# Performance work log

Measured on AMD Instinct MI355X. Metric: run time of the kernel, lower is better.

Reference implementation:

```python
import jax, jax.numpy as jnp
import numpy as np

N, LQ, C, M, L, P = 8, 2048, 256, 8, 4, 4
DH = C // M  # 32
LENS = (2048, 1024, 512, 256)


def setup_inputs() -> dict:
    key = jax.random.key(0)
    ks = jax.random.split(key, 8)
    s = 1.0 / np.sqrt(C)
    return {
        "query": jax.random.normal(ks[0], (N, LQ, C), jnp.float32),
        "reference_points": jax.random.uniform(ks[1], (N, LQ, L, 1), jnp.float32),
        "input_flatten": jax.random.normal(ks[2], (N, sum(LENS), C), jnp.float32),
        "temporal_lens": np.array(LENS, np.int64),
        "level_start_index": np.array([0, 2048, 3072, 3584], np.int64),
        "W_off": jax.random.normal(ks[3], (C, M * L * P), jnp.float32) * 0.01,
        "b_off": jax.random.normal(ks[4], (M * L * P,), jnp.float32),
        "W_attn": jax.random.normal(ks[5], (C, M * L * P), jnp.float32) * 0.01,
        "b_attn": jnp.zeros((M * L * P,), jnp.float32),
        "W_val": jax.random.normal(ks[6], (C, C), jnp.float32) * s,
        "b_val": jnp.zeros((C,), jnp.float32),
        "W_out": jax.random.normal(ks[7], (C, C), jnp.float32) * s,
        "b_out": jnp.zeros((C,), jnp.float32),
    }


def _deform_core(value, lens, loc, attn):
    # value: (N, S, M, DH); loc, attn: (N, LQ, M, L, P); loc in normalized [0,1] coords.
    # Equivalent to per-level F.grid_sample (bilinear, zeros padding, align_corners=False)
    # on a 1xT image: pixel position = loc*T - 0.5; the y-coord 0.5 lands exactly on row 0.
    outs = []
    start = 0
    for l, T in enumerate(lens):
        v = value[:, start:start + T].transpose(0, 2, 1, 3)  # (N, M, T, DH)
        start += T
        pos = loc[..., l, :] * T - 0.5                       # (N, LQ, M, P)
        x0f = jnp.floor(pos)
        frac = pos - x0f
        x0 = x0f.astype(jnp.int32)

        def gather(idx):
            i = jnp.clip(idx, 0, T - 1).transpose(0, 2, 1, 3).reshape(N, M, LQ * P, 1)
            return jnp.take_along_axis(v, i, axis=2).reshape(N, M, LQ, P, DH)

        in0 = ((x0 >= 0) & (x0 < T)).astype(value.dtype)
        in1 = ((x0 + 1 >= 0) & (x0 + 1 < T)).astype(value.dtype)
        w0 = ((1.0 - frac) * in0).transpose(0, 2, 1, 3)[..., None]  # (N, M, LQ, P, 1)
        w1 = (frac * in1).transpose(0, 2, 1, 3)[..., None]
        outs.append(gather(x0) * w0 + gather(x0 + 1) * w1)          # (N, M, LQ, P, DH)
    sampled = jnp.stack(outs, axis=3)          # (N, M, LQ, L, P, DH)
    aw = attn.transpose(0, 2, 1, 3, 4)         # (N, M, LQ, L, P)
    return jnp.einsum('nmqlpd,nmqlp->nqmd', sampled, aw).reshape(N, LQ, C)


def reference(query, reference_points, input_flatten, temporal_lens, level_start_index,
              W_off, b_off, W_attn, b_attn, W_val, b_val, W_out, b_out):
    lens = [int(t) for t in np.asarray(temporal_lens)[:L]]  # static per-level lengths
    value = (input_flatten @ W_val + b_val).reshape(N, -1, M, DH)
    off = (query @ W_off + b_off).reshape(N, LQ, M, L, P)
    attn = jax.nn.softmax((query @ W_attn + b_attn).reshape(N, LQ, M, L * P), axis=-1)
    attn = attn.reshape(N, LQ, M, L, P)
    norm = jnp.asarray(lens, query.dtype)                    # offset_normalizer (L,)
    loc = reference_points[:, :, None, :, None, 0] + off / norm[None, None, None, :, None]
    out = _deform_core(value, lens, loc, attn)
    out = out @ W_out + b_out
    return out, loc, attn
```

## Files before the change

kernel.cpp:

```cpp
#include <hip/hip_runtime.h>
#include <hip/hip_bf16.h>
#include <math.h>

#define NB 8
#define LQ 2048
#define CCH 256
#define SSUM 3840

typedef unsigned short ushort_t;
typedef unsigned int uint_t;
typedef __attribute__((ext_vector_type(8))) short bf16x8;
typedef __attribute__((ext_vector_type(4))) float f32x4;

__device__ inline ushort_t f2bf(float f) {
  __hip_bfloat16 h = __float2bfloat16(f);
  return *reinterpret_cast<ushort_t*>(&h);
}
__device__ inline uint_t pk2bf(float lo, float hi) {
  float2 t; t.x = lo; t.y = hi;
  __hip_bfloat162 h = __float22bfloat162_rn(t);
  return *reinterpret_cast<uint_t*>(&h);
}
__device__ inline float bf2f_lo(uint_t u) {
  union { uint_t u32; float f; } x;
  x.u32 = u << 16;
  return x.f;
}
__device__ inline float bf2f_hi(uint_t u) {
  union { uint_t u32; float f; } x;
  x.u32 = u & 0xffff0000u;
  return x.f;
}

__global__ __launch_bounds__(256) void gemm_multi(
    int job_base,
    const float* __restrict__ in_flat, const float* __restrict__ query,
    const ushort_t* __restrict__ core,
    const float* __restrict__ W_val, const float* __restrict__ W_off,
    const float* __restrict__ W_attn, const float* __restrict__ W_out,
    const float* __restrict__ b_val, const float* __restrict__ b_off,
    const float* __restrict__ b_attn, const float* __restrict__ b_out,
    ushort_t* __restrict__ value, float* __restrict__ loc,
    float* __restrict__ attn, float* __restrict__ out) {
  __shared__ ushort_t Abf[2][128][24];
  __shared__ ushort_t Bbf[2][128][24];

  const int job = job_base + blockIdx.x;

  const float* Af = nullptr;
  const ushort_t* Ab16 = nullptr;
  const float* W; const float* bias;
  int wstride, wcol, bm, cstride, colbase;
  float* Cf = nullptr; ushort_t* Cb = nullptr;

  if (job < 480) {
    int bn = (job & 1) * 128; bm = (job >> 1) * 128;
    Af = in_flat; W = W_val; wstride = 256; wcol = bn;
    bias = b_val + bn; Cb = value; cstride = 256; colbase = bn;
  } else if (job < 736) {
    int p = job - 480; bm = (p >> 1) * 128;
    Af = query;
    if (p & 1) { W = W_attn; bias = b_attn; Cf = attn; }
    else       { W = W_off;  bias = b_off;  Cf = loc;  }
    wstride = 128; wcol = 0; cstride = 128; colbase = 0;
  } else {
    int o = job - 736; int bn = (o & 1) * 128; bm = (o >> 1) * 128;
    Ab16 = core; W = W_out; wstride = 256; wcol = bn;
    bias = b_out + bn; Cf = out; cstride = 256; colbase = bn;
  }

  const int tid = threadIdx.x;
  const int lane = tid & 63;
  const int wv = tid >> 6;
  const int wm = (wv >> 1) * 64;
  const int wn = (wv & 1) * 64;
  const int quad = lane >> 4;
  const int l16 = lane & 15;
  const int sr = tid & 127;
  const int sh = tid >> 7;
  const int kq = tid >> 5;
  const int ln = tid & 31;

  f32x4 acc[4][4];
#pragma unroll
  for (int i = 0; i < 4; ++i)
#pragma unroll
    for (int j = 0; j < 4; ++j) acc[i][j] = (f32x4)(0.f);

  for (int k0 = 0; k0 < 256; k0 += 32) {
    uint4 aq0, aq1;
    if (Af) {
      const float* gp = Af + (size_t)(bm + sr) * 256 + k0 + sh * 16;
      float4 f0 = *(const float4*)(gp + 0);
      float4 f1 = *(const float4*)(gp + 4);
      float4 f2 = *(const float4*)(gp + 8);
      float4 f3 = *(const float4*)(gp + 12);
      aq0.x = pk2bf(f0.x, f0.y); aq0.y = pk2bf(f0.z, f0.w);
      aq0.z = pk2bf(f1.x, f1.y); aq0.w = pk2bf(f1.z, f1.w);
      aq1.x = pk2bf(f2.x, f2.y); aq1.y = pk2bf(f2.z, f2.w);
      aq1.z = pk2bf(f3.x, f3.y); aq1.w = pk2bf(f3.z, f3.w);
    } else {
      const ushort_t* gp = Ab16 + (size_t)(bm + sr) * 256 + k0 + sh * 16;
      aq0 = *(const uint4*)(gp + 0);
      aq1 = *(const uint4*)(gp + 8);
    }
    float wreg[16];
#pragma unroll
    for (int j = 0; j < 4; ++j) {
      const float* wp = W + (size_t)(k0 + kq + j * 8) * wstride + wcol + ln;
#pragma unroll
      for (int nb = 0; nb < 4; ++nb) wreg[j * 4 + nb] = wp[nb * 32];
    }

    __syncthreads();
    *(uint4*)&Abf[sh][sr][0] = aq0;
    *(uint4*)&Abf[sh][sr][8] = aq1;
#pragma unroll
    for (int j = 0; j < 4; ++j) {
      int k = kq + j * 8;
#pragma unroll
      for (int nb = 0; nb < 4; ++nb)
        Bbf[k >> 4][ln + nb * 32][k & 15] = f2bf(wreg[j * 4 + nb]);
    }
    __syncthreads();

    bf16x8 af[4], bfr[4];
#pragma unroll
    for (int mi = 0; mi < 4; ++mi)
      af[mi] = *(const bf16x8*)&Abf[quad >> 1][wm + mi * 16 + l16][(quad & 1) * 8];
#pragma unroll
    for (int ni = 0; ni < 4; ++ni)
      bfr[ni] = *(const bf16x8*)&Bbf[quad >> 1][wn + ni * 16 + l16][(quad & 1) * 8];
#pragma unroll
    for (int mi = 0; mi < 4; ++mi)
#pragma unroll
      for (int ni = 0; ni < 4; ++ni)
        acc[mi][ni] = __builtin_amdgcn_mfma_f32_16x16x32_bf16(af[mi], bfr[ni], acc[mi][ni], 0, 0, 0);
  }

#pragma unroll
  for (int ni = 0; ni < 4; ++ni) {
    int cc = wn + ni * 16 + l16;
    float bv = bias[cc];
#pragma unroll
    for (int mi = 0; mi < 4; ++mi) {
      f32x4 v = acc[mi][ni];
      int rbase = bm + wm + mi * 16 + quad * 4;
#pragma unroll
      for (int r = 0; r < 4; ++r) {
        float o = v[r] + bv;
        size_t idx = (size_t)(rbase + r) * cstride + colbase + cc;
        if (Cb) Cb[idx] = f2bf(o);
        else    Cf[idx] = o;
      }
    }
  }
}

__global__ __launch_bounds__(256) void deform_fused(
    const ushort_t* __restrict__ value,
    float* __restrict__ locbuf,
    float* __restrict__ attnbuf,
    const float* __restrict__ refp,
    ushort_t* __restrict__ core) {
  const int tid = threadIdx.x;
  const int nq0 = blockIdx.x * 4;
  const int n = nq0 >> 11;

  __shared__ float slv[512];
  __shared__ float slog[512];
  __shared__ float4 sp[512];

  const float rnorm[4] = {1.f / 2048.f, 1.f / 1024.f, 1.f / 512.f, 1.f / 256.f};
  const int lensA[4] = {2048, 1024, 512, 256};
  const int startsA[4] = {0, 2048, 3072, 3584};

#pragma unroll
  for (int j = 0; j < 2; ++j) {
    int s = tid + j * 256;
    int q = s >> 7;
    int r = s & 127;
    int l = (r >> 2) & 3;
    float lv = refp[(size_t)(nq0 + q) * 4 + l] +
               locbuf[(size_t)nq0 * 128 + s] * rnorm[l];
    locbuf[(size_t)nq0 * 128 + s] = lv;
    slv[s] = lv;
    slog[s] = attnbuf[(size_t)nq0 * 128 + s];
  }
  __syncthreads();

  if (tid < 32) {
    int base = tid * 16;
    float v[16];
#pragma unroll
    for (int i = 0; i < 16; ++i) v[i] = slog[base + i];
    float mx = v[0];
#pragma unroll
    for (int i = 1; i < 16; ++i) mx = fmaxf(mx, v[i]);
    float ssum = 0.f;
#pragma unroll
    for (int i = 0; i < 16; ++i) { v[i] = __expf(v[i] - mx); ssum += v[i]; }
    float rs = 1.f / ssum;
    float* gout = attnbuf + (size_t)nq0 * 128 + base;
#pragma unroll
    for (int i = 0; i < 16; ++i) {
      float pv = v[i] * rs;
      slog[base + i] = pv;
      gout[i] = pv;
    }
  }
  __syncthreads();

#pragma unroll
  for (int j = 0; j < 2; ++j) {
    int s = tid + j * 256;
    int q = s >> 7;
    int r = s & 127;
    int m = r >> 4;
    int lp = r & 15;
    int l = lp >> 2;
    int T = lensA[l];
    float lv = slv[s];
    float aw = slog[s];
    float pos = lv * (float)T - 0.5f;
    float x0f = floorf(pos);
    float fr = pos - x0f;
    int x0 = (int)x0f;
    float w0 = ((unsigned)x0 < (unsigned)T) ? (1.f - fr) * aw : 0.f;
    float w1 = ((unsigned)(x0 + 1) < (unsigned)T) ? fr * aw : 0.f;
    int i0 = min(max(x0, 0), T - 1);
    int i1 = min(max(x0 + 1, 0), T - 1);
    float4 pr;
    pr.x = w0;
    pr.y = w1;
    pr.z = __int_as_float((startsA[l] + i0) * 256);
    pr.w = __int_as_float((startsA[l] + i1) * 256);
    sp[q * 128 + lp * 8 + m] = pr;
  }
  __syncthreads();

  const int q = tid >> 6;
  const int t64 = tid & 63;
  const int m = t64 >> 3;
  const int g = t64 & 7;
  const ushort_t* vbase = value + (size_t)n * (SSUM * 256) + m * 32 + g * 4;

  float a0 = 0.f, a1 = 0.f, a2 = 0.f, a3 = 0.f;
#pragma unroll
  for (int lp = 0; lp < 16; ++lp) {
    float4 pr = sp[q * 128 + lp * 8 + m];
    int o0 = __float_as_int(pr.z);
    int o1 = __float_as_int(pr.w);
    uint2 u0 = *(const uint2*)(vbase + o0);
    uint2 u1 = *(const uint2*)(vbase + o1);
    a0 += pr.x * bf2f_lo(u0.x) + pr.y * bf2f_lo(u1.x);
    a1 += pr.x * bf2f_hi(u0.x) + pr.y * bf2f_hi(u1.x);
    a2 += pr.x * bf2f_lo(u0.y) + pr.y * bf2f_lo(u1.y);
    a3 += pr.x * bf2f_hi(u0.y) + pr.y * bf2f_hi(u1.y);
  }
  uint2 outp;
  outp.x = (uint_t)f2bf(a0) | ((uint_t)f2bf(a1) << 16);
  outp.y = (uint_t)f2bf(a2) | ((uint_t)f2bf(a3) << 16);
  *(uint2*)&core[(size_t)(nq0 + q) * 256 + m * 32 + g * 4] = outp;
}

extern "C" void kernel_launch(void* const* d_in, const int* in_sizes, int n_in,
                              void* d_out, int out_size, void* d_ws, size_t ws_size,
                              hipStream_t stream) {
  const float* query    = (const float*)d_in[0];
  const float* refpts   = (const float*)d_in[1];
  const float* in_flat  = (const float*)d_in[2];
  const float* W_off  = (const float*)d_in[5];
  const float* b_off  = (const float*)d_in[6];
  const float* W_attn = (const float*)d_in[7];
  const float* b_attn = (const float*)d_in[8];
  const float* W_val  = (const float*)d_in[9];
  const float* b_val  = (const float*)d_in[10];
  const float* W_out  = (const float*)d_in[11];
  const float* b_out  = (const float*)d_in[12];

  float* out  = (float*)d_out;
  float* loc  = out + (size_t)NB * LQ * CCH;
  float* attn = loc + (size_t)NB * LQ * 128;

  ushort_t* value = (ushort_t*)d_ws;
  ushort_t* core  = value + (size_t)NB * SSUM * CCH;

  const int Mq = NB * LQ;

  gemm_multi<<<736, 256, 0, stream>>>(
      0, in_flat, query, core, W_val, W_off, W_attn, W_out,
      b_val, b_off, b_attn, b_out, value, loc, attn, out);

  deform_fused<<<Mq / 4, 256, 0, stream>>>(value, loc, attn, refpts, core);

  gemm_multi<<<256, 256, 0, stream>>>(
      736, in_flat, query, core, W_val, W_off, W_attn, W_out,
      b_val, b_off, b_attn, b_out, value, loc, attn, out);
}
```

Before: 180.9 us.

## Pre-convert inputs and weights to bf16, use async global-to-LDS double-buffered GEMM

Adds a prologue kernel that converts in_flat and query to bf16 and writes transposed bf16 copies of all weight matrices. The GEMM kernel is replaced by one that streams bf16 tiles straight into LDS with global_load_lds, double-buffered, using a 64x128 tile in place of 128x128. The aim is to drop the in-loop fp32 loads, conversions and strided weight reads and to overlap loads with MFMA. The cost is an extra launch and an extra full read and write pass over the activations, and the core buffer now aliases the query_bf buffer.

```diff
diff --git a/kernel.cpp b/kernel.cpp
--- a/kernel.cpp
+++ b/kernel.cpp
@@ -4,7 +4,6 @@
 
 #define NB 8
 #define LQ 2048
-#define CCH 256
 #define SSUM 3840
 
 typedef unsigned short ushort_t;
@@ -12,127 +11,132 @@
 typedef __attribute__((ext_vector_type(8))) short bf16x8;
 typedef __attribute__((ext_vector_type(4))) float f32x4;
 
-__device__ inline ushort_t f2bf(float f) {
+__device__ __forceinline__ ushort_t f2bf(float f) {
   __hip_bfloat16 h = __float2bfloat16(f);
   return *reinterpret_cast<ushort_t*>(&h);
 }
-__device__ inline uint_t pk2bf(float lo, float hi) {
+__device__ __forceinline__ uint_t pk2bf(float lo, float hi) {
   float2 t; t.x = lo; t.y = hi;
   __hip_bfloat162 h = __float22bfloat162_rn(t);
   return *reinterpret_cast<uint_t*>(&h);
 }
-__device__ inline float bf2f_lo(uint_t u) {
+__device__ __forceinline__ float bf2f_lo(uint_t u) {
   union { uint_t u32; float f; } x;
   x.u32 = u << 16;
   return x.f;
 }
-__device__ inline float bf2f_hi(uint_t u) {
+__device__ __forceinline__ float bf2f_hi(uint_t u) {
   union { uint_t u32; float f; } x;
   x.u32 = u & 0xffff0000u;
   return x.f;
 }
-
-__global__ __launch_bounds__(256) void gemm_multi(
-    int job_base,
+__device__ __forceinline__ void ld_lds16(const void* g, void* l) {
+  __builtin_amdgcn_global_load_lds(
+      (const __attribute__((address_space(1))) void*)g,
+      (__attribute__((address_space(3))) void*)l, 16, 0, 0);
+}
+
+#define NF4A ((NB * SSUM * 256) / 4)
+#define NF4B ((NB * LQ * 256) / 4)
+
+__global__ __launch_bounds__(256) void prologue(
     const float* __restrict__ in_flat, const float* __restrict__ query,
-    const ushort_t* __restrict__ core,
     const float* __restrict__ W_val, const float* __restrict__ W_off,
     const float* __restrict__ W_attn, const float* __restrict__ W_out,
+    ushort_t* __restrict__ inflat_bf, ushort_t* __restrict__ query_bf,
+    ushort_t* __restrict__ BtVal, ushort_t* __restrict__ BtOA,
+    ushort_t* __restrict__ BtOut) {
+  const int b = blockIdx.x, t = threadIdx.x;
+  if (b < 256) { BtVal[b * 256 + t] = f2bf(W_val[(size_t)t * 256 + b]); return; }
+  if (b < 512) { int n = b - 256; BtOut[n * 256 + t] = f2bf(W_out[(size_t)t * 256 + n]); return; }
+  if (b < 640) { int n = b - 512; BtOA[n * 256 + t] = f2bf(W_off[(size_t)t * 128 + n]); return; }
+  if (b < 768) { int n = b - 640; BtOA[(128 + n) * 256 + t] = f2bf(W_attn[(size_t)t * 128 + n]); return; }
+  const int stride = (gridDim.x - 768) * 256;
+  for (int i = (b - 768) * 256 + t; i < NF4A + NF4B; i += stride) {
+    float4 v;
+    if (i < NF4A) v = ((const float4*)in_flat)[i];
+    else          v = ((const float4*)query)[i - NF4A];
+    uint2 o;
+    o.x = pk2bf(v.x, v.y);
+    o.y = pk2bf(v.z, v.w);
+    if (i < NF4A) *(uint2*)&inflat_bf[(size_t)i * 4] = o;
+    else          *(uint2*)&query_bf[(size_t)(i - NF4A) * 4] = o;
+  }
+}
+
+__global__ __launch_bounds__(256) void gemm_async(
+    int job_base,
+    const ushort_t* __restrict__ inflat_bf, const ushort_t* __restrict__ query_bf,
+    const ushort_t* __restrict__ core,
+    const ushort_t* __restrict__ BtVal, const ushort_t* __restrict__ BtOA,
+    const ushort_t* __restrict__ BtOut,
     const float* __restrict__ b_val, const float* __restrict__ b_off,
     const float* __restrict__ b_attn, const float* __restrict__ b_out,
     ushort_t* __restrict__ value, float* __restrict__ loc,
     float* __restrict__ attn, float* __restrict__ out) {
-  __shared__ ushort_t Abf[2][128][24];
-  __shared__ ushort_t Bbf[2][128][24];
+  __shared__ ushort_t Ab[2][64][32];
+  __shared__ ushort_t Bb[2][128][32];
 
   const int job = job_base + blockIdx.x;
 
-  const float* Af = nullptr;
-  const ushort_t* Ab16 = nullptr;
-  const float* W; const float* bias;
-  int wstride, wcol, bm, cstride, colbase;
-  float* Cf = nullptr; ushort_t* Cb = nullptr;
-
-  if (job < 480) {
-    int bn = (job & 1) * 128; bm = (job >> 1) * 128;
-    Af = in_flat; W = W_val; wstride = 256; wcol = bn;
-    bias = b_val + bn; Cb = value; cstride = 256; colbase = bn;
-  } else if (job < 736) {
-    int p = job - 480; bm = (p >> 1) * 128;
-    Af = query;
-    if (p & 1) { W = W_attn; bias = b_attn; Cf = attn; }
-    else       { W = W_off;  bias = b_off;  Cf = loc;  }
-    wstride = 128; wcol = 0; cstride = 128; colbase = 0;
+  const ushort_t* Asrc; const ushort_t* Bt; const float* bias;
+  int bm, colbase, cstride;
+  ushort_t* Cb = nullptr; float* Cf = nullptr;
+
+  if (job < 960) {
+    int cn = job & 1; bm = (job >> 1) * 64;
+    Asrc = inflat_bf; Bt = BtVal + cn * 128 * 256;
+    bias = b_val + cn * 128; Cb = value; cstride = 256; colbase = cn * 128;
+  } else if (job < 1472) {
+    int p = job - 960; int cn = p & 1; bm = (p >> 1) * 64;
+    Asrc = query_bf; Bt = BtOA + cn * 128 * 256;
+    bias = cn ? b_attn : b_off; Cf = cn ? attn : loc; cstride = 128; colbase = 0;
   } else {
-    int o = job - 736; int bn = (o & 1) * 128; bm = (o >> 1) * 128;
-    Ab16 = core; W = W_out; wstride = 256; wcol = bn;
-    bias = b_out + bn; Cf = out; cstride = 256; colbase = bn;
+    int o = job - 1472; int cn = o & 1; bm = (o >> 1) * 64;
+    Asrc = core; Bt = BtOut + cn * 128 * 256;
+    bias = b_out + cn * 128; Cf = out; cstride = 256; colbase = cn * 128;
   }
 
   const int tid = threadIdx.x;
   const int lane = tid & 63;
   const int wv = tid >> 6;
-  const int wm = (wv >> 1) * 64;
-  const int wn = (wv & 1) * 64;
   const int quad = lane >> 4;
   const int l16 = lane & 15;
-  const int sr = tid & 127;
-  const int sh = tid >> 7;
-  const int kq = tid >> 5;
-  const int ln = tid & 31;
-
-  f32x4 acc[4][4];
-#pragma unroll
-  for (int i = 0; i < 4; ++i)
+  const int wm = (wv >> 1) * 32;
+  const int wn = (wv & 1) * 64;
+  const int srow = lane >> 2;
+  const int skb = (lane & 3) * 8;
+
+  f32x4 acc[2][4];
+#pragma unroll
+  for (int i = 0; i < 2; ++i)
 #pragma unroll
     for (int j = 0; j < 4; ++j) acc[i][j] = (f32x4)(0.f);
 
-  for (int k0 = 0; k0 < 256; k0 += 32) {
-    uint4 aq0, aq1;
-    if (Af) {
-      const float* gp = Af + (size_t)(bm + sr) * 256 + k0 + sh * 16;
-      float4 f0 = *(const float4*)(gp + 0);
-      float4 f1 = *(const float4*)(gp + 4);
-      float4 f2 = *(const float4*)(gp + 8);
-      float4 f3 = *(const float4*)(gp + 12);
-      aq0.x = pk2bf(f0.x, f0.y); aq0.y = pk2bf(f0.z, f0.w);
-      aq0.z = pk2bf(f1.x, f1.y); aq0.w = pk2bf(f1.z, f1.w);
-      aq1.x = pk2bf(f2.x, f2.y); aq1.y = pk2bf(f2.z, f2.w);
-      aq1.z = pk2bf(f3.x, f3.y); aq1.w = pk2bf(f3.z, f3.w);
-    } else {
-      const ushort_t* gp = Ab16 + (size_t)(bm + sr) * 256 + k0 + sh * 16;
-      aq0 = *(const uint4*)(gp + 0);
-      aq1 = *(const uint4*)(gp + 8);
-    }
-    float wreg[16];
-#pragma unroll
-    for (int j = 0; j < 4; ++j) {
-      const float* wp = W + (size_t)(k0 + kq + j * 8) * wstride + wcol + ln;
-#pragma unroll
-      for (int nb = 0; nb < 4; ++nb) wreg[j * 4 + nb] = wp[nb * 32];
-    }
-
+  auto stage = [&](int db, int k0) {
+    ld_lds16(Asrc + (size_t)(bm + wv * 16 + srow) * 256 + k0 + skb,
+             &Ab[db][wv * 16 + srow][skb]);
+    ld_lds16(Bt + (size_t)(wv * 32 + srow) * 256 + k0 + skb,
+             &Bb[db][wv * 32 + srow][skb]);
+    ld_lds16(Bt + (size_t)(wv * 32 + 16 + srow) * 256 + k0 + skb,
+             &Bb[db][wv * 32 + 16 + srow][skb]);
+  };
+
+  stage(0, 0);
+#pragma unroll
+  for (int it = 0; it < 8; ++it) {
+    const int db = it & 1;
     __syncthreads();
-    *(uint4*)&Abf[sh][sr][0] = aq0;
-    *(uint4*)&Abf[sh][sr][8] = aq1;
-#pragma unroll
-    for (int j = 0; j < 4; ++j) {
-      int k = kq + j * 8;
-#pragma unroll
-      for (int nb = 0; nb < 4; ++nb)
-        Bbf[k >> 4][ln + nb * 32][k & 15] = f2bf(wreg[j * 4 + nb]);
-    }
-    __syncthreads();
-
-    bf16x8 af[4], bfr[4];
-#pragma unroll
-    for (int mi = 0; mi < 4; ++mi)
-      af[mi] = *(const bf16x8*)&Abf[quad >> 1][wm + mi * 16 + l16][(quad & 1) * 8];
+    if (it < 7) stage(db ^ 1, (it + 1) * 32);
+    bf16x8 af[2], bfr[4];
+#pragma unroll
+    for (int mi = 0; mi < 2; ++mi)
+      af[mi] = *(const bf16x8*)&Ab[db][wm + mi * 16 + l16][quad * 8];
 #pragma unroll
     for (int ni = 0; ni < 4; ++ni)
-      bfr[ni] = *(const bf16x8*)&Bbf[quad >> 1][wn + ni * 16 + l16][(quad & 1) * 8];
-#pragma unroll
-    for (int mi = 0; mi < 4; ++mi)
+      bfr[ni] = *(const bf16x8*)&Bb[db][wn + ni * 16 + l16][quad * 8];
+#pragma unroll
+    for (int mi = 0; mi < 2; ++mi)
 #pragma unroll
       for (int ni = 0; ni < 4; ++ni)
         acc[mi][ni] = __builtin_amdgcn_mfma_f32_16x16x32_bf16(af[mi], bfr[ni], acc[mi][ni], 0, 0, 0);
@@ -140,16 +144,17 @@
 
 #pragma unroll
   for (int ni = 0; ni < 4; ++ni) {
-    int cc = wn + ni * 16 + l16;
-    float bv = bias[cc];
-#pragma unroll
-    for (int mi = 0; mi < 4; ++mi) {
+    int lc = wn + ni * 16 + l16;
+    float bv = bias[lc];
+    int cc = colbase + lc;
+#pragma unroll
+    for (int mi = 0; mi < 2; ++mi) {
       f32x4 v = acc[mi][ni];
       int rbase = bm + wm + mi * 16 + quad * 4;
 #pragma unroll
       for (int r = 0; r < 4; ++r) {
         float o = v[r] + bv;
-        size_t idx = (size_t)(rbase + r) * cstride + colbase + cc;
+        size_t idx = (size_t)(rbase + r) * cstride + cc;
         if (Cb) Cb[idx] = f2bf(o);
         else    Cf[idx] = o;
       }
@@ -280,21 +285,30 @@
   const float* b_out  = (const float*)d_in[12];
 
   float* out  = (float*)d_out;
-  float* loc  = out + (size_t)NB * LQ * CCH;
+  float* loc  = out + (size_t)NB * LQ * 256;
   float* attn = loc + (size_t)NB * LQ * 128;
 
-  ushort_t* value = (ushort_t*)d_ws;
-  ushort_t* core  = value + (size_t)NB * SSUM * CCH;
+  ushort_t* value     = (ushort_t*)d_ws;
+  ushort_t* inflat_bf = value + (size_t)NB * SSUM * 256;
+  ushort_t* query_bf  = inflat_bf + (size_t)NB * SSUM * 256;
+  ushort_t* core      = query_bf;
+  ushort_t* BtVal     = query_bf + (size_t)NB * LQ * 256;
+  ushort_t* BtOA      = BtVal + 65536;
+  ushort_t* BtOut     = BtOA + 65536;
 
   const int Mq = NB * LQ;
 
-  gemm_multi<<<736, 256, 0, stream>>>(
-      0, in_flat, query, core, W_val, W_off, W_attn, W_out,
+  prologue<<<768 + 2048, 256, 0, stream>>>(
+      in_flat, query, W_val, W_off, W_attn, W_out,
+      inflat_bf, query_bf, BtVal, BtOA, BtOut);
+
+  gemm_async<<<1472, 256, 0, stream>>>(
+      0, inflat_bf, query_bf, core, BtVal, BtOA, BtOut,
       b_val, b_off, b_attn, b_out, value, loc, attn, out);
 
   deform_fused<<<Mq / 4, 256, 0, stream>>>(value, loc, attn, refpts, core);
 
-  gemm_multi<<<256, 256, 0, stream>>>(
-      736, in_flat, query, core, W_val, W_off, W_attn, W_out,
+  gemm_async<<<512, 256, 0, stream>>>(
+      1472, inflat_bf, query_bf, core, BtVal, BtOA, BtOut,
       b_val, b_off, b_attn, b_out, value, loc, attn, out);
 }
```

Result: faster. 174.5 us (-3.5%).
